# Kernel optimization log

Hardware: AMD Instinct MI355X
Metric: run time of the kernel (lower is better)

Reference implementation:

```python
import jax, jax.numpy as jnp
import numpy as np

N_NODES = 50000
N_EDGES = 800000
IN_DIM = 128
HID = 64
NUM_GRAPHS = 64


def _gcn_conv(x, W, b, src, dst, num_nodes):
    """PyG GCNConv: out = D^-1/2 (A+I) D^-1/2 (x W) + b, messages scattered to dst."""
    h = x @ W  # [N, out]
    ones = jnp.ones((src.shape[0],), dtype=x.dtype)
    # degree at target nodes, self-loop adds 1
    deg = jax.ops.segment_sum(ones, dst, num_segments=num_nodes) + 1.0
    dinv = jax.lax.rsqrt(deg)  # [N]
    norm = dinv[src] * dinv[dst]  # [E]
    msgs = h[src] * norm[:, None]  # [E, out] gather-scale
    agg = jax.ops.segment_sum(msgs, dst, num_segments=num_nodes)  # scatter-add
    # self-loop contribution: norm_ii = dinv[i]^2
    agg = agg + h * (dinv * dinv)[:, None]
    return agg + b


def setup_inputs() -> dict:
    key = jax.random.key(0)
    k = jax.random.split(key, 10)
    x = jax.random.normal(k[0], (N_NODES, IN_DIM), dtype=jnp.float32)
    edge_index = jax.random.randint(k[1], (2, N_EDGES), 0, N_NODES, dtype=jnp.int32)
    batch = jnp.sort(jax.random.randint(k[2], (N_NODES,), 0, NUM_GRAPHS, dtype=jnp.int32))
    # Glorot-ish params
    W1 = jax.random.normal(k[3], (IN_DIM, HID), dtype=jnp.float32) / np.sqrt(IN_DIM)
    b1 = jnp.zeros((HID,), dtype=jnp.float32)
    W2 = jax.random.normal(k[4], (HID, HID), dtype=jnp.float32) / np.sqrt(HID)
    b2 = jnp.zeros((HID,), dtype=jnp.float32)
    Wlin = jax.random.normal(k[5], (HID, 1), dtype=jnp.float32) / np.sqrt(HID)
    blin = jnp.zeros((1,), dtype=jnp.float32)
    return {"x": x, "edge_index": edge_index, "batch": batch,
            "W1": W1, "b1": b1, "W2": W2, "b2": b2, "Wlin": Wlin, "blin": blin}


def reference(x, edge_index, batch, W1, b1, W2, b2, Wlin, blin):
    src, dst = edge_index[0], edge_index[1]
    h = _gcn_conv(x, W1, b1, src, dst, N_NODES)
    h = jax.nn.relu(h)  # dropout is identity in eval mode
    h = _gcn_conv(h, W2, b2, src, dst, N_NODES)
    h = jax.nn.relu(h)
    # global mean pool per graph
    sums = jax.ops.segment_sum(h, batch, num_segments=NUM_GRAPHS)  # [G, HID]
    cnts = jax.ops.segment_sum(jnp.ones((N_NODES,), h.dtype), batch, num_segments=NUM_GRAPHS)
    pooled = sums / jnp.maximum(cnts, 1.0)[:, None]
    return pooled @ Wlin + blin  # [G, 1]
```

## Files before the change

kernel.cpp:

```cpp
#include <hip/hip_runtime.h>
#include <hip/hip_fp16.h>

#define N_NODES 50000
#define N_EDGES 800000
#define IN_DIM 128
#define HID 64
#define NUM_GRAPHS 64
#define NB 196
#define NBLK 64

__device__ inline float4 load_h4(const __half* p) {
    const __half2* q = (const __half2*)p;
    float2 a = __half22float2(q[0]);
    float2 b = __half22float2(q[1]);
    return make_float4(a.x, a.y, b.x, b.y);
}
__device__ inline void store_h4(__half* p, float4 v) {
    __half2* q = (__half2*)p;
    q[0] = __floats2half2_rn(v.x, v.y);
    q[1] = __floats2half2_rn(v.z, v.w);
}
__device__ inline void load_h8(const __half* p, float* f) {
    float4 r = *(const float4*)p;
    const __half2* h = (const __half2*)&r;
    float2 a0 = __half22float2(h[0]);
    float2 a1 = __half22float2(h[1]);
    float2 a2 = __half22float2(h[2]);
    float2 a3 = __half22float2(h[3]);
    f[0] = a0.x; f[1] = a0.y; f[2] = a1.x; f[3] = a1.y;
    f[4] = a2.x; f[5] = a2.y; f[6] = a3.x; f[7] = a3.y;
}
__device__ inline void store_h8(__half* p, const float* f) {
    __half2 hs[4];
    hs[0] = __floats2half2_rn(f[0], f[1]);
    hs[1] = __floats2half2_rn(f[2], f[3]);
    hs[2] = __floats2half2_rn(f[4], f[5]);
    hs[3] = __floats2half2_rn(f[6], f[7]);
    *(float4*)p = *(const float4*)hs;
}

__global__ __launch_bounds__(256) void hist_kernel(const int* __restrict__ dst, int* __restrict__ hist_g) {
    __shared__ int h[NB];
    int tid = threadIdx.x;
    for (int i = tid; i < NB; i += 256) h[i] = 0;
    __syncthreads();
    const int NI = N_EDGES / 4;
    for (int i = blockIdx.x * 256 + tid; i < NI; i += NBLK * 256) {
        int4 d = ((const int4*)dst)[i];
        atomicAdd(&h[d.x >> 8], 1);
        atomicAdd(&h[d.y >> 8], 1);
        atomicAdd(&h[d.z >> 8], 1);
        atomicAdd(&h[d.w >> 8], 1);
    }
    __syncthreads();
    for (int i = tid; i < NB; i += 256) hist_g[i * NBLK + blockIdx.x] = h[i];
}

__global__ __launch_bounds__(1024) void scan2_kernel(const int* __restrict__ in, int* __restrict__ pos,
                                                     int* __restrict__ offs) {
    __shared__ int wsum[16];
    __shared__ int tot_s;
    int tid = threadIdx.x;
    int lane = tid & 63, wid = tid >> 6;
    int carry = 0;
    const int L = NB * NBLK;
    for (int base = 0; base < L; base += 4096) {
        int idx = base + tid * 4;
        int v0 = 0, v1 = 0, v2 = 0, v3 = 0;
        if (idx < L) { int4 v = *(const int4*)&in[idx]; v0 = v.x; v1 = v.y; v2 = v.z; v3 = v.w; }
        int s0 = v0, s1 = s0 + v1, s2 = s1 + v2, s3 = s2 + v3;
        int inc = s3;
        #pragma unroll
        for (int d = 1; d < 64; d <<= 1) { int t = __shfl_up(inc, d, 64); if (lane >= d) inc += t; }
        if (lane == 63) wsum[wid] = inc;
        __syncthreads();
        if (tid < 16) {
            int wv = wsum[tid], winc = wv;
            #pragma unroll
            for (int d = 1; d < 16; d <<= 1) { int t = __shfl_up(winc, d, 16); if (tid >= d) winc += t; }
            wsum[tid] = winc - wv;
            if (tid == 15) tot_s = winc;
        }
        __syncthreads();
        int excl = carry + wsum[wid] + inc - s3;
        if (idx < L) { int4 o; o.x = excl; o.y = excl + s0; o.z = excl + s1; o.w = excl + s2; *(int4*)&pos[idx] = o; }
        carry += tot_s;
    }
    if (tid == 0) offs[N_NODES] = N_EDGES;
}

__global__ __launch_bounds__(256) void bin_kernel(const int* __restrict__ src, const int* __restrict__ dst,
                                                  const int* __restrict__ pos, int* __restrict__ binned) {
    __shared__ int cur[NB];
    int tid = threadIdx.x;
    for (int i = tid; i < NB; i += 256) cur[i] = pos[i * NBLK + blockIdx.x];
    __syncthreads();
    const int NI = N_EDGES / 4;
    for (int i = blockIdx.x * 256 + tid; i < NI; i += NBLK * 256) {
        int4 s = ((const int4*)src)[i];
        int4 d = ((const int4*)dst)[i];
        int p0 = atomicAdd(&cur[d.x >> 8], 1); binned[p0] = (s.x & 0xFFFF) | ((d.x & 255) << 16);
        int p1 = atomicAdd(&cur[d.y >> 8], 1); binned[p1] = (s.y & 0xFFFF) | ((d.y & 255) << 16);
        int p2 = atomicAdd(&cur[d.z >> 8], 1); binned[p2] = (s.z & 0xFFFF) | ((d.z & 255) << 16);
        int p3 = atomicAdd(&cur[d.w >> 8], 1); binned[p3] = (s.w & 0xFFFF) | ((d.w & 255) << 16);
    }
}

__global__ __launch_bounds__(256) void build_kernel(const int* __restrict__ binned, const int* __restrict__ pos,
                                                    int* __restrict__ offs, float* __restrict__ dinv,
                                                    unsigned short* __restrict__ csr_src) {
    __shared__ int cnt[256];
    __shared__ int excl[256];
    __shared__ int rnk[256];
    __shared__ int wtot[4];
    int b = blockIdx.x, tid = threadIdx.x;
    int base = pos[b * NBLK];
    int end  = (b == NB - 1) ? N_EDGES : pos[(b + 1) * NBLK];
    cnt[tid] = 0; rnk[tid] = 0;
    __syncthreads();
    for (int j = base + tid; j < end; j += 256) atomicAdd(&cnt[(binned[j] >> 16) & 255], 1);
    __syncthreads();
    int v = cnt[tid];
    int lane = tid & 63, wid = tid >> 6;
    int inc = v;
    #pragma unroll
    for (int d = 1; d < 64; d <<= 1) { int t = __shfl_up(inc, d, 64); if (lane >= d) inc += t; }
    if (lane == 63) wtot[wid] = inc;
    __syncthreads();
    if (tid == 0) {
        int a = 0;
        for (int w = 0; w < 4; w++) { int t = wtot[w]; wtot[w] = a; a += t; }
    }
    __syncthreads();
    excl[tid] = wtot[wid] + inc - v;
    int node = b * 256 + tid;
    if (node < N_NODES) {
        offs[node] = base + excl[tid];
        dinv[node] = rsqrtf((float)v + 1.0f);
    }
    __syncthreads();
    for (int j = base + tid; j < end; j += 256) {
        int e = binned[j];
        int l = (e >> 16) & 255;
        int r = atomicAdd(&rnk[l], 1);
        csr_src[base + excl[l] + r] = (unsigned short)(e & 0xFFFF);
    }
}

template <int K, typename TIN>
__global__ __launch_bounds__(256) void gemm_kernel(const TIN* __restrict__ A, const float* __restrict__ W,
                                                   const float* __restrict__ dinv,
                                                   __half* __restrict__ out, int nRows) {
    constexpr int KB = 64;
    constexpr int KBP = KB + 4;
    __shared__ float xs[64 * KBP];
    __shared__ float ws[KB * 68];
    int tid = threadIdx.x;
    int node0 = blockIdx.x * 64;
    int c0 = (tid & 15) * 4, n0 = (tid >> 4) * 4;
    float acc[4][4] = {};
    for (int kb = 0; kb < K; kb += KB) {
        for (int i = tid; i < KB * 16; i += 256) {
            int k = i >> 4, c4 = (i & 15) * 4;
            *(float4*)&ws[k * 68 + c4] = *(const float4*)&W[(size_t)(kb + k) * 64 + c4];
        }
        for (int i = tid; i < 64 * (KB / 4); i += 256) {
            int n = i / (KB / 4), k4 = (i % (KB / 4)) * 4;
            int gn = node0 + n;
            float4 v;
            if (gn < nRows) {
                if constexpr (sizeof(TIN) == 4) v = *(const float4*)&A[(size_t)gn * K + kb + k4];
                else                            v = load_h4((const __half*)&A[(size_t)gn * K + kb + k4]);
            } else v = make_float4(0.f, 0.f, 0.f, 0.f);
            *(float4*)&xs[n * KBP + k4] = v;
        }
        __syncthreads();
        for (int k = 0; k < KB; k += 4) {
            float4 x0 = *(const float4*)&xs[(n0 + 0) * KBP + k];
            float4 x1 = *(const float4*)&xs[(n0 + 1) * KBP + k];
            float4 x2 = *(const float4*)&xs[(n0 + 2) * KBP + k];
            float4 x3 = *(const float4*)&xs[(n0 + 3) * KBP + k];
            #define KSTEP(KK, F) { \
                float4 wr = *(const float4*)&ws[(k + KK) * 68 + c0]; \
                acc[0][0] += x0.F * wr.x; acc[0][1] += x0.F * wr.y; acc[0][2] += x0.F * wr.z; acc[0][3] += x0.F * wr.w; \
                acc[1][0] += x1.F * wr.x; acc[1][1] += x1.F * wr.y; acc[1][2] += x1.F * wr.z; acc[1][3] += x1.F * wr.w; \
                acc[2][0] += x2.F * wr.x; acc[2][1] += x2.F * wr.y; acc[2][2] += x2.F * wr.z; acc[2][3] += x2.F * wr.w; \
                acc[3][0] += x3.F * wr.x; acc[3][1] += x3.F * wr.y; acc[3][2] += x3.F * wr.z; acc[3][3] += x3.F * wr.w; }
            KSTEP(0, x)
            KSTEP(1, y)
            KSTEP(2, z)
            KSTEP(3, w)
            #undef KSTEP
        }
        __syncthreads();
    }
    #pragma unroll
    for (int i = 0; i < 4; i++) {
        int gn = node0 + n0 + i;
        if (gn < nRows) {
            float sc = dinv[gn];
            store_h4(&out[(size_t)gn * 64 + c0],
                     make_float4(acc[i][0] * sc, acc[i][1] * sc, acc[i][2] * sc, acc[i][3] * sc));
        }
    }
}

__global__ __launch_bounds__(256) void agg_kernel(const __half* __restrict__ hd, const int* __restrict__ offs,
                                                  const unsigned short* __restrict__ csr_src,
                                                  const float* __restrict__ dinv, const float* __restrict__ bias,
                                                  __half* __restrict__ out) {
    int lane = threadIdx.x & 63;
    int node = blockIdx.x * 4 + (threadIdx.x >> 6);
    if (node >= N_NODES) return;
    int g = lane >> 3;
    int cc = (lane & 7) * 8;
    float acc[8] = {};
    int beg = offs[node], end = offs[node + 1];
    #pragma unroll 2
    for (int j = beg + g; j < end; j += 8) {
        int s = csr_src[j];
        float hv[8];
        load_h8(&hd[(size_t)s * 64 + cc], hv);
        #pragma unroll
        for (int i = 0; i < 8; i++) acc[i] += hv[i];
    }
    #pragma unroll
    for (int m = 8; m <= 32; m <<= 1) {
        #pragma unroll
        for (int i = 0; i < 8; i++) acc[i] += __shfl_xor(acc[i], m, 64);
    }
    if (g == 0) {
        float di = dinv[node];
        float hn[8];
        load_h8(&hd[(size_t)node * 64 + cc], hn);
        float4 bv0 = *(const float4*)&bias[cc];
        float4 bv1 = *(const float4*)&bias[cc + 4];
        float bb[8] = {bv0.x, bv0.y, bv0.z, bv0.w, bv1.x, bv1.y, bv1.z, bv1.w};
        float r[8];
        #pragma unroll
        for (int i = 0; i < 8; i++) r[i] = fmaxf(fmaf(di, acc[i] + hn[i], bb[i]), 0.0f);
        store_h8(&out[(size_t)node * 64 + cc], r);
    }
}

__global__ __launch_bounds__(256) void agg2dot_kernel(const __half* __restrict__ hd, const int* __restrict__ offs,
                                                      const unsigned short* __restrict__ csr_src,
                                                      const float* __restrict__ dinv, const float* __restrict__ bias,
                                                      const float* __restrict__ Wlin,
                                                      float* __restrict__ ndot) {
    int lane = threadIdx.x & 63;
    int node = blockIdx.x * 4 + (threadIdx.x >> 6);
    if (node >= N_NODES) return;
    int g = lane >> 3;
    int cc = (lane & 7) * 8;
    float acc[8] = {};
    int beg = offs[node], end = offs[node + 1];
    #pragma unroll 2
    for (int j = beg + g; j < end; j += 8) {
        int s = csr_src[j];
        float hv[8];
        load_h8(&hd[(size_t)s * 64 + cc], hv);
        #pragma unroll
        for (int i = 0; i < 8; i++) acc[i] += hv[i];
    }
    #pragma unroll
    for (int m = 8; m <= 32; m <<= 1) {
        #pragma unroll
        for (int i = 0; i < 8; i++) acc[i] += __shfl_xor(acc[i], m, 64);
    }
    if (g == 0) {
        float di = dinv[node];
        float hn[8];
        load_h8(&hd[(size_t)node * 64 + cc], hn);
        float4 bv0 = *(const float4*)&bias[cc];
        float4 bv1 = *(const float4*)&bias[cc + 4];
        float bb[8] = {bv0.x, bv0.y, bv0.z, bv0.w, bv1.x, bv1.y, bv1.z, bv1.w};
        float4 wl0 = *(const float4*)&Wlin[cc];
        float4 wl1 = *(const float4*)&Wlin[cc + 4];
        float ww[8] = {wl0.x, wl0.y, wl0.z, wl0.w, wl1.x, wl1.y, wl1.z, wl1.w};
        float d = 0.0f;
        #pragma unroll
        for (int i = 0; i < 8; i++) {
            float r = fmaxf(fmaf(di, acc[i] + hn[i], bb[i]), 0.0f);
            d = fmaf(r, ww[i], d);
        }
        #pragma unroll
        for (int m = 1; m < 8; m <<= 1) d += __shfl_xor(d, m, 64);
        if ((lane & 7) == 0) ndot[node] = d;
    }
}

__global__ __launch_bounds__(256) void graphred_kernel(const float* __restrict__ ndot, const int* __restrict__ batch,
                                                       const float* __restrict__ blin, float* __restrict__ out) {
    __shared__ float wpart[4];
    int g = blockIdx.x;
    int tid = threadIdx.x;
    int lo = 0, hi = N_NODES;
    while (lo < hi) { int m = (lo + hi) >> 1; if (batch[m] < g) lo = m + 1; else hi = m; }
    int lo2 = lo, hi2 = N_NODES;
    while (lo2 < hi2) { int m = (lo2 + hi2) >> 1; if (batch[m] < g + 1) lo2 = m + 1; else hi2 = m; }
    float s = 0.0f;
    for (int i = lo + tid; i < lo2; i += 256) s += ndot[i];
    int lane = tid & 63, wid = tid >> 6;
    #pragma unroll
    for (int m = 32; m > 0; m >>= 1) s += __shfl_down(s, m, 64);
    if (lane == 0) wpart[wid] = s;
    __syncthreads();
    if (tid == 0) {
        float t = wpart[0] + wpart[1] + wpart[2] + wpart[3];
        float cnt = (float)(lo2 - lo);
        out[g] = t / fmaxf(cnt, 1.0f) + blin[0];
    }
}

extern "C" void kernel_launch(void* const* d_in, const int* in_sizes, int n_in,
                              void* d_out, int out_size, void* d_ws, size_t ws_size,
                              hipStream_t stream) {
    const float* x    = (const float*)d_in[0];
    const int*   ei   = (const int*)d_in[1];
    const int*   batch= (const int*)d_in[2];
    const float* W1   = (const float*)d_in[3];
    const float* b1   = (const float*)d_in[4];
    const float* W2   = (const float*)d_in[5];
    const float* b2   = (const float*)d_in[6];
    const float* Wlin = (const float*)d_in[7];
    const float* blin = (const float*)d_in[8];
    float* out = (float*)d_out;
    const int* srcA = ei;
    const int* dstA = ei + N_EDGES;

    char* p = (char*)d_ws;
    auto alloc = [&](size_t n) { char* r = p; p += (n + 255) & ~(size_t)255; return r; };
    int*    hist_g  = (int*)alloc((size_t)NB * NBLK * 4);
    int*    pos     = (int*)alloc((size_t)NB * NBLK * 4);
    int*    offs    = (int*)alloc((size_t)(N_NODES + 1) * 4);
    int*    binned  = (int*)alloc((size_t)N_EDGES * 4);
    unsigned short* csr_src = (unsigned short*)alloc((size_t)N_EDGES * 2);
    float*  dinv    = (float*)alloc((size_t)N_NODES * 4);
    float*  ndot    = (float*)alloc((size_t)N_NODES * 4);
    __half* bufA    = (__half*)alloc((size_t)N_NODES * 64 * 2);
    __half* bufB    = (__half*)alloc((size_t)N_NODES * 64 * 2);

    hist_kernel<<<NBLK, 256, 0, stream>>>(dstA, hist_g);
    scan2_kernel<<<1, 1024, 0, stream>>>(hist_g, pos, offs);
    bin_kernel<<<NBLK, 256, 0, stream>>>(srcA, dstA, pos, binned);
    build_kernel<<<NB, 256, 0, stream>>>(binned, pos, offs, dinv, csr_src);

    gemm_kernel<IN_DIM, float><<<(N_NODES + 63) / 64, 256, 0, stream>>>(x, W1, dinv, bufA, N_NODES);
    agg_kernel<<<(N_NODES + 3) / 4, 256, 0, stream>>>(bufA, offs, csr_src, dinv, b1, bufB);
    gemm_kernel<HID, __half><<<(N_NODES + 63) / 64, 256, 0, stream>>>(bufB, W2, dinv, bufA, N_NODES);
    agg2dot_kernel<<<(N_NODES + 3) / 4, 256, 0, stream>>>(bufA, offs, csr_src, dinv, b2, Wlin, ndot);

    graphred_kernel<<<NUM_GRAPHS, 256, 0, stream>>>(ndot, batch, blin, out);
}
```

Baseline: 206.8 us.

## Fuse graph-build, GEMM1, scan/bin and pooling kernels to cut launches

Runs the dst histogram, the per-graph node counts and the first GEMM as branches of one kernel, dropping the dinv pre-scaling so GEMM1 no longer waits on the degree build; dinv[src] is applied per edge in the first aggregation instead. Each of the 64 binning blocks now computes the full hist scan redundantly in shared memory, which removes the single-block scan launch. Graph pooling moves into the second aggregation kernel through slotted float atomics and a last-block-arrives reduction, which removes the separate graph-reduction kernel. The costs are an extra per-edge dinv gather, a 50 KB shared-memory load in every binning block, and atomic contention on the pooling slots.

```diff
diff --git a/kernel.cpp b/kernel.cpp
--- a/kernel.cpp
+++ b/kernel.cpp
@@ -8,6 +8,7 @@
 #define NUM_GRAPHS 64
 #define NB 196
 #define NBLK 64
+#define NSLOT 32
 
 __device__ inline float4 load_h4(const __half* p) {
     const __half2* q = (const __half2*)p;
@@ -39,147 +40,34 @@
     *(float4*)p = *(const float4*)hs;
 }
 
-__global__ __launch_bounds__(256) void hist_kernel(const int* __restrict__ dst, int* __restrict__ hist_g) {
-    __shared__ int h[NB];
+template <int K, typename TIN, bool SCALE>
+__device__ __forceinline__ void gemm_body(const TIN* __restrict__ A, const float* __restrict__ W,
+                                          const float* __restrict__ dinv, __half* __restrict__ out,
+                                          int nRows, int node0, float* xs, float* ws) {
     int tid = threadIdx.x;
-    for (int i = tid; i < NB; i += 256) h[i] = 0;
-    __syncthreads();
-    const int NI = N_EDGES / 4;
-    for (int i = blockIdx.x * 256 + tid; i < NI; i += NBLK * 256) {
-        int4 d = ((const int4*)dst)[i];
-        atomicAdd(&h[d.x >> 8], 1);
-        atomicAdd(&h[d.y >> 8], 1);
-        atomicAdd(&h[d.z >> 8], 1);
-        atomicAdd(&h[d.w >> 8], 1);
-    }
-    __syncthreads();
-    for (int i = tid; i < NB; i += 256) hist_g[i * NBLK + blockIdx.x] = h[i];
-}
-
-__global__ __launch_bounds__(1024) void scan2_kernel(const int* __restrict__ in, int* __restrict__ pos,
-                                                     int* __restrict__ offs) {
-    __shared__ int wsum[16];
-    __shared__ int tot_s;
-    int tid = threadIdx.x;
-    int lane = tid & 63, wid = tid >> 6;
-    int carry = 0;
-    const int L = NB * NBLK;
-    for (int base = 0; base < L; base += 4096) {
-        int idx = base + tid * 4;
-        int v0 = 0, v1 = 0, v2 = 0, v3 = 0;
-        if (idx < L) { int4 v = *(const int4*)&in[idx]; v0 = v.x; v1 = v.y; v2 = v.z; v3 = v.w; }
-        int s0 = v0, s1 = s0 + v1, s2 = s1 + v2, s3 = s2 + v3;
-        int inc = s3;
-        #pragma unroll
-        for (int d = 1; d < 64; d <<= 1) { int t = __shfl_up(inc, d, 64); if (lane >= d) inc += t; }
-        if (lane == 63) wsum[wid] = inc;
-        __syncthreads();
-        if (tid < 16) {
-            int wv = wsum[tid], winc = wv;
-            #pragma unroll
-            for (int d = 1; d < 16; d <<= 1) { int t = __shfl_up(winc, d, 16); if (tid >= d) winc += t; }
-            wsum[tid] = winc - wv;
-            if (tid == 15) tot_s = winc;
-        }
-        __syncthreads();
-        int excl = carry + wsum[wid] + inc - s3;
-        if (idx < L) { int4 o; o.x = excl; o.y = excl + s0; o.z = excl + s1; o.w = excl + s2; *(int4*)&pos[idx] = o; }
-        carry += tot_s;
-    }
-    if (tid == 0) offs[N_NODES] = N_EDGES;
-}
-
-__global__ __launch_bounds__(256) void bin_kernel(const int* __restrict__ src, const int* __restrict__ dst,
-                                                  const int* __restrict__ pos, int* __restrict__ binned) {
-    __shared__ int cur[NB];
-    int tid = threadIdx.x;
-    for (int i = tid; i < NB; i += 256) cur[i] = pos[i * NBLK + blockIdx.x];
-    __syncthreads();
-    const int NI = N_EDGES / 4;
-    for (int i = blockIdx.x * 256 + tid; i < NI; i += NBLK * 256) {
-        int4 s = ((const int4*)src)[i];
-        int4 d = ((const int4*)dst)[i];
-        int p0 = atomicAdd(&cur[d.x >> 8], 1); binned[p0] = (s.x & 0xFFFF) | ((d.x & 255) << 16);
-        int p1 = atomicAdd(&cur[d.y >> 8], 1); binned[p1] = (s.y & 0xFFFF) | ((d.y & 255) << 16);
-        int p2 = atomicAdd(&cur[d.z >> 8], 1); binned[p2] = (s.z & 0xFFFF) | ((d.z & 255) << 16);
-        int p3 = atomicAdd(&cur[d.w >> 8], 1); binned[p3] = (s.w & 0xFFFF) | ((d.w & 255) << 16);
-    }
-}
-
-__global__ __launch_bounds__(256) void build_kernel(const int* __restrict__ binned, const int* __restrict__ pos,
-                                                    int* __restrict__ offs, float* __restrict__ dinv,
-                                                    unsigned short* __restrict__ csr_src) {
-    __shared__ int cnt[256];
-    __shared__ int excl[256];
-    __shared__ int rnk[256];
-    __shared__ int wtot[4];
-    int b = blockIdx.x, tid = threadIdx.x;
-    int base = pos[b * NBLK];
-    int end  = (b == NB - 1) ? N_EDGES : pos[(b + 1) * NBLK];
-    cnt[tid] = 0; rnk[tid] = 0;
-    __syncthreads();
-    for (int j = base + tid; j < end; j += 256) atomicAdd(&cnt[(binned[j] >> 16) & 255], 1);
-    __syncthreads();
-    int v = cnt[tid];
-    int lane = tid & 63, wid = tid >> 6;
-    int inc = v;
-    #pragma unroll
-    for (int d = 1; d < 64; d <<= 1) { int t = __shfl_up(inc, d, 64); if (lane >= d) inc += t; }
-    if (lane == 63) wtot[wid] = inc;
-    __syncthreads();
-    if (tid == 0) {
-        int a = 0;
-        for (int w = 0; w < 4; w++) { int t = wtot[w]; wtot[w] = a; a += t; }
-    }
-    __syncthreads();
-    excl[tid] = wtot[wid] + inc - v;
-    int node = b * 256 + tid;
-    if (node < N_NODES) {
-        offs[node] = base + excl[tid];
-        dinv[node] = rsqrtf((float)v + 1.0f);
-    }
-    __syncthreads();
-    for (int j = base + tid; j < end; j += 256) {
-        int e = binned[j];
-        int l = (e >> 16) & 255;
-        int r = atomicAdd(&rnk[l], 1);
-        csr_src[base + excl[l] + r] = (unsigned short)(e & 0xFFFF);
-    }
-}
-
-template <int K, typename TIN>
-__global__ __launch_bounds__(256) void gemm_kernel(const TIN* __restrict__ A, const float* __restrict__ W,
-                                                   const float* __restrict__ dinv,
-                                                   __half* __restrict__ out, int nRows) {
-    constexpr int KB = 64;
-    constexpr int KBP = KB + 4;
-    __shared__ float xs[64 * KBP];
-    __shared__ float ws[KB * 68];
-    int tid = threadIdx.x;
-    int node0 = blockIdx.x * 64;
     int c0 = (tid & 15) * 4, n0 = (tid >> 4) * 4;
     float acc[4][4] = {};
-    for (int kb = 0; kb < K; kb += KB) {
-        for (int i = tid; i < KB * 16; i += 256) {
+    for (int kb = 0; kb < K; kb += 64) {
+        for (int i = tid; i < 64 * 16; i += 256) {
             int k = i >> 4, c4 = (i & 15) * 4;
             *(float4*)&ws[k * 68 + c4] = *(const float4*)&W[(size_t)(kb + k) * 64 + c4];
         }
-        for (int i = tid; i < 64 * (KB / 4); i += 256) {
-            int n = i / (KB / 4), k4 = (i % (KB / 4)) * 4;
+        for (int i = tid; i < 64 * 16; i += 256) {
+            int n = i >> 4, k4 = (i & 15) * 4;
             int gn = node0 + n;
             float4 v;
             if (gn < nRows) {
                 if constexpr (sizeof(TIN) == 4) v = *(const float4*)&A[(size_t)gn * K + kb + k4];
                 else                            v = load_h4((const __half*)&A[(size_t)gn * K + kb + k4]);
             } else v = make_float4(0.f, 0.f, 0.f, 0.f);
-            *(float4*)&xs[n * KBP + k4] = v;
-        }
-        __syncthreads();
-        for (int k = 0; k < KB; k += 4) {
-            float4 x0 = *(const float4*)&xs[(n0 + 0) * KBP + k];
-            float4 x1 = *(const float4*)&xs[(n0 + 1) * KBP + k];
-            float4 x2 = *(const float4*)&xs[(n0 + 2) * KBP + k];
-            float4 x3 = *(const float4*)&xs[(n0 + 3) * KBP + k];
+            *(float4*)&xs[n * 68 + k4] = v;
+        }
+        __syncthreads();
+        for (int k = 0; k < 64; k += 4) {
+            float4 x0 = *(const float4*)&xs[(n0 + 0) * 68 + k];
+            float4 x1 = *(const float4*)&xs[(n0 + 1) * 68 + k];
+            float4 x2 = *(const float4*)&xs[(n0 + 2) * 68 + k];
+            float4 x3 = *(const float4*)&xs[(n0 + 3) * 68 + k];
             #define KSTEP(KK, F) { \
                 float4 wr = *(const float4*)&ws[(k + KK) * 68 + c0]; \
                 acc[0][0] += x0.F * wr.x; acc[0][1] += x0.F * wr.y; acc[0][2] += x0.F * wr.z; acc[0][3] += x0.F * wr.w; \
@@ -198,20 +86,147 @@
     for (int i = 0; i < 4; i++) {
         int gn = node0 + n0 + i;
         if (gn < nRows) {
-            float sc = dinv[gn];
+            float sc = 1.0f;
+            if constexpr (SCALE) sc = dinv[gn];
             store_h4(&out[(size_t)gn * 64 + c0],
                      make_float4(acc[i][0] * sc, acc[i][1] * sc, acc[i][2] * sc, acc[i][3] * sc));
         }
     }
 }
 
-__global__ __launch_bounds__(256) void agg_kernel(const __half* __restrict__ hd, const int* __restrict__ offs,
-                                                  const unsigned short* __restrict__ csr_src,
-                                                  const float* __restrict__ dinv, const float* __restrict__ bias,
-                                                  __half* __restrict__ out) {
+__global__ __launch_bounds__(256) void k1_kernel(const int* __restrict__ dst, int* __restrict__ hist_g,
+                                                 const float* __restrict__ x, const float* __restrict__ W1,
+                                                 __half* __restrict__ h1,
+                                                 const int* __restrict__ batch, float* __restrict__ gsum,
+                                                 int* __restrict__ gcnt, int* __restrict__ arrive) {
+    __shared__ __align__(16) float smem[2 * 64 * 68];
+    int blk = blockIdx.x, tid = threadIdx.x;
+    if (blk < NBLK) {
+        int* h = (int*)smem;
+        for (int i = tid; i < NB; i += 256) h[i] = 0;
+        __syncthreads();
+        const int NI = N_EDGES / 4;
+        for (int i = blk * 256 + tid; i < NI; i += NBLK * 256) {
+            int4 d = ((const int4*)dst)[i];
+            atomicAdd(&h[d.x >> 8], 1);
+            atomicAdd(&h[d.y >> 8], 1);
+            atomicAdd(&h[d.z >> 8], 1);
+            atomicAdd(&h[d.w >> 8], 1);
+        }
+        __syncthreads();
+        for (int i = tid; i < NB; i += 256) hist_g[i * NBLK + blk] = h[i];
+    } else if (blk == NBLK) {
+        int* c = (int*)smem;
+        if (tid < NUM_GRAPHS) c[tid] = 0;
+        for (int i = tid; i < NSLOT * NUM_GRAPHS; i += 256) gsum[i] = 0.0f;
+        if (tid == 0) arrive[0] = 0;
+        __syncthreads();
+        const int4* b4 = (const int4*)batch;
+        for (int i = tid; i < N_NODES / 4; i += 256) {
+            int4 v = b4[i];
+            atomicAdd(&c[v.x], 1); atomicAdd(&c[v.y], 1);
+            atomicAdd(&c[v.z], 1); atomicAdd(&c[v.w], 1);
+        }
+        __syncthreads();
+        if (tid < NUM_GRAPHS) gcnt[tid] = c[tid];
+    } else {
+        int node0 = (blk - NBLK - 1) * 64;
+        gemm_body<IN_DIM, float, false>(x, W1, nullptr, h1, N_NODES, node0, smem, smem + 64 * 68);
+    }
+}
+
+__global__ __launch_bounds__(256) void k2_binscan(const int* __restrict__ hist_g,
+                                                  const int* __restrict__ src, const int* __restrict__ dst,
+                                                  int* __restrict__ binned, int* __restrict__ bstart,
+                                                  int* __restrict__ offs) {
+    __shared__ int ld[NB * NBLK];
+    __shared__ int cur[NB];
+    __shared__ int wsum[4];
+    int tid = threadIdx.x, blk = blockIdx.x;
+    for (int i = tid; i < NB * NBLK; i += 256) ld[i] = hist_g[i];
+    __syncthreads();
+    const int CH = (NB * NBLK) / 256;
+    int base = tid * CH;
+    int s = 0;
+    for (int k = 0; k < CH; k++) { int v = ld[base + k]; ld[base + k] = s; s += v; }
+    int lane = tid & 63, wid = tid >> 6;
+    int inc = s;
+    #pragma unroll
+    for (int d = 1; d < 64; d <<= 1) { int t = __shfl_up(inc, d, 64); if (lane >= d) inc += t; }
+    if (lane == 63) wsum[wid] = inc;
+    __syncthreads();
+    if (tid == 0) {
+        int a = 0;
+        for (int w = 0; w < 4; w++) { int t = wsum[w]; wsum[w] = a; a += t; }
+    }
+    __syncthreads();
+    int off = wsum[wid] + inc - s;
+    for (int k = 0; k < CH; k++) ld[base + k] += off;
+    __syncthreads();
+    for (int b = tid; b < NB; b += 256) cur[b] = ld[b * NBLK + blk];
+    if (blk == 0) {
+        for (int b = tid; b < NB; b += 256) bstart[b] = ld[b * NBLK];
+        if (tid == 0) { bstart[NB] = N_EDGES; offs[N_NODES] = N_EDGES; }
+    }
+    __syncthreads();
+    const int NI = N_EDGES / 4;
+    for (int i = blk * 256 + tid; i < NI; i += NBLK * 256) {
+        int4 sv = ((const int4*)src)[i];
+        int4 dv = ((const int4*)dst)[i];
+        int p0 = atomicAdd(&cur[dv.x >> 8], 1); binned[p0] = (sv.x & 0xFFFF) | ((dv.x & 255) << 16);
+        int p1 = atomicAdd(&cur[dv.y >> 8], 1); binned[p1] = (sv.y & 0xFFFF) | ((dv.y & 255) << 16);
+        int p2 = atomicAdd(&cur[dv.z >> 8], 1); binned[p2] = (sv.z & 0xFFFF) | ((dv.z & 255) << 16);
+        int p3 = atomicAdd(&cur[dv.w >> 8], 1); binned[p3] = (sv.w & 0xFFFF) | ((dv.w & 255) << 16);
+    }
+}
+
+__global__ __launch_bounds__(256) void build_kernel(const int* __restrict__ binned, const int* __restrict__ bstart,
+                                                    int* __restrict__ offs, float* __restrict__ dinv,
+                                                    unsigned short* __restrict__ csr_src) {
+    __shared__ int cnt[256];
+    __shared__ int excl[256];
+    __shared__ int rnk[256];
+    __shared__ int wtot[4];
+    int b = blockIdx.x, tid = threadIdx.x;
+    int base = bstart[b];
+    int end  = bstart[b + 1];
+    cnt[tid] = 0; rnk[tid] = 0;
+    __syncthreads();
+    for (int j = base + tid; j < end; j += 256) atomicAdd(&cnt[(binned[j] >> 16) & 255], 1);
+    __syncthreads();
+    int v = cnt[tid];
+    int lane = tid & 63, wid = tid >> 6;
+    int inc = v;
+    #pragma unroll
+    for (int d = 1; d < 64; d <<= 1) { int t = __shfl_up(inc, d, 64); if (lane >= d) inc += t; }
+    if (lane == 63) wtot[wid] = inc;
+    __syncthreads();
+    if (tid == 0) {
+        int a = 0;
+        for (int w = 0; w < 4; w++) { int t = wtot[w]; wtot[w] = a; a += t; }
+    }
+    __syncthreads();
+    excl[tid] = wtot[wid] + inc - v;
+    int node = b * 256 + tid;
+    if (node < N_NODES) {
+        offs[node] = base + excl[tid];
+        dinv[node] = rsqrtf((float)v + 1.0f);
+    }
+    __syncthreads();
+    for (int j = base + tid; j < end; j += 256) {
+        int e = binned[j];
+        int l = (e >> 16) & 255;
+        int r = atomicAdd(&rnk[l], 1);
+        csr_src[base + excl[l] + r] = (unsigned short)(e & 0xFFFF);
+    }
+}
+
+__global__ __launch_bounds__(256) void agg1_kernel(const __half* __restrict__ hd, const int* __restrict__ offs,
+                                                   const unsigned short* __restrict__ csr_src,
+                                                   const float* __restrict__ dinv, const float* __restrict__ bias,
+                                                   __half* __restrict__ out) {
     int lane = threadIdx.x & 63;
     int node = blockIdx.x * 4 + (threadIdx.x >> 6);
-    if (node >= N_NODES) return;
     int g = lane >> 3;
     int cc = (lane & 7) * 8;
     float acc[8] = {};
@@ -219,10 +234,11 @@
     #pragma unroll 2
     for (int j = beg + g; j < end; j += 8) {
         int s = csr_src[j];
+        float dv = dinv[s];
         float hv[8];
         load_h8(&hd[(size_t)s * 64 + cc], hv);
         #pragma unroll
-        for (int i = 0; i < 8; i++) acc[i] += hv[i];
+        for (int i = 0; i < 8; i++) acc[i] = fmaf(hv[i], dv, acc[i]);
     }
     #pragma unroll
     for (int m = 8; m <= 32; m <<= 1) {
@@ -231,6 +247,7 @@
     }
     if (g == 0) {
         float di = dinv[node];
+        float d2 = di * di;
         float hn[8];
         load_h8(&hd[(size_t)node * 64 + cc], hn);
         float4 bv0 = *(const float4*)&bias[cc];
@@ -238,19 +255,27 @@
         float bb[8] = {bv0.x, bv0.y, bv0.z, bv0.w, bv1.x, bv1.y, bv1.z, bv1.w};
         float r[8];
         #pragma unroll
-        for (int i = 0; i < 8; i++) r[i] = fmaxf(fmaf(di, acc[i] + hn[i], bb[i]), 0.0f);
+        for (int i = 0; i < 8; i++) r[i] = fmaxf(fmaf(di, acc[i], fmaf(d2, hn[i], bb[i])), 0.0f);
         store_h8(&out[(size_t)node * 64 + cc], r);
     }
 }
 
-__global__ __launch_bounds__(256) void agg2dot_kernel(const __half* __restrict__ hd, const int* __restrict__ offs,
+__global__ __launch_bounds__(256) void gemm2_kernel(const __half* __restrict__ A, const float* __restrict__ W,
+                                                    const float* __restrict__ dinv, __half* __restrict__ out) {
+    __shared__ __align__(16) float smem[2 * 64 * 68];
+    gemm_body<HID, __half, true>(A, W, dinv, out, N_NODES, blockIdx.x * 64, smem, smem + 64 * 68);
+}
+
+__global__ __launch_bounds__(256) void agg2red_kernel(const __half* __restrict__ hd, const int* __restrict__ offs,
                                                       const unsigned short* __restrict__ csr_src,
                                                       const float* __restrict__ dinv, const float* __restrict__ bias,
-                                                      const float* __restrict__ Wlin,
-                                                      float* __restrict__ ndot) {
+                                                      const float* __restrict__ Wlin, const int* __restrict__ batch,
+                                                      float* __restrict__ gsum, const int* __restrict__ gcnt,
+                                                      int* __restrict__ arrive, const float* __restrict__ blin,
+                                                      float* __restrict__ out) {
+    __shared__ int is_last;
     int lane = threadIdx.x & 63;
     int node = blockIdx.x * 4 + (threadIdx.x >> 6);
-    if (node >= N_NODES) return;
     int g = lane >> 3;
     int cc = (lane & 7) * 8;
     float acc[8] = {};
@@ -286,30 +311,25 @@
         }
         #pragma unroll
         for (int m = 1; m < 8; m <<= 1) d += __shfl_xor(d, m, 64);
-        if ((lane & 7) == 0) ndot[node] = d;
-    }
-}
-
-__global__ __launch_bounds__(256) void graphred_kernel(const float* __restrict__ ndot, const int* __restrict__ batch,
-                                                       const float* __restrict__ blin, float* __restrict__ out) {
-    __shared__ float wpart[4];
-    int g = blockIdx.x;
-    int tid = threadIdx.x;
-    int lo = 0, hi = N_NODES;
-    while (lo < hi) { int m = (lo + hi) >> 1; if (batch[m] < g) lo = m + 1; else hi = m; }
-    int lo2 = lo, hi2 = N_NODES;
-    while (lo2 < hi2) { int m = (lo2 + hi2) >> 1; if (batch[m] < g + 1) lo2 = m + 1; else hi2 = m; }
-    float s = 0.0f;
-    for (int i = lo + tid; i < lo2; i += 256) s += ndot[i];
-    int lane = tid & 63, wid = tid >> 6;
-    #pragma unroll
-    for (int m = 32; m > 0; m >>= 1) s += __shfl_down(s, m, 64);
-    if (lane == 0) wpart[wid] = s;
-    __syncthreads();
-    if (tid == 0) {
-        float t = wpart[0] + wpart[1] + wpart[2] + wpart[3];
-        float cnt = (float)(lo2 - lo);
-        out[g] = t / fmaxf(cnt, 1.0f) + blin[0];
+        if (lane == 0) {
+            int gb = batch[node];
+            atomicAdd(&gsum[(blockIdx.x & (NSLOT - 1)) * NUM_GRAPHS + gb], d);
+        }
+    }
+    __syncthreads();
+    if (threadIdx.x == 0) {
+        __threadfence();
+        int old = atomicAdd(arrive, 1);
+        is_last = (old == (int)gridDim.x - 1) ? 1 : 0;
+    }
+    __syncthreads();
+    if (is_last && threadIdx.x < NUM_GRAPHS) {
+        int gg = threadIdx.x;
+        float s = 0.0f;
+        #pragma unroll
+        for (int slot = 0; slot < NSLOT; slot++) s += atomicAdd(&gsum[slot * NUM_GRAPHS + gg], 0.0f);
+        float cnt = (float)gcnt[gg];
+        out[gg] = s / fmaxf(cnt, 1.0f) + blin[0];
     }
 }
 
@@ -332,24 +352,24 @@
     char* p = (char*)d_ws;
     auto alloc = [&](size_t n) { char* r = p; p += (n + 255) & ~(size_t)255; return r; };
     int*    hist_g  = (int*)alloc((size_t)NB * NBLK * 4);
-    int*    pos     = (int*)alloc((size_t)NB * NBLK * 4);
+    int*    bstart  = (int*)alloc((size_t)(NB + 1) * 4);
     int*    offs    = (int*)alloc((size_t)(N_NODES + 1) * 4);
     int*    binned  = (int*)alloc((size_t)N_EDGES * 4);
     unsigned short* csr_src = (unsigned short*)alloc((size_t)N_EDGES * 2);
     float*  dinv    = (float*)alloc((size_t)N_NODES * 4);
-    float*  ndot    = (float*)alloc((size_t)N_NODES * 4);
+    float*  gsum    = (float*)alloc((size_t)NSLOT * NUM_GRAPHS * 4);
+    int*    gcnt    = (int*)alloc((size_t)NUM_GRAPHS * 4);
+    int*    arrive  = (int*)alloc(4);
     __half* bufA    = (__half*)alloc((size_t)N_NODES * 64 * 2);
     __half* bufB    = (__half*)alloc((size_t)N_NODES * 64 * 2);
 
-    hist_kernel<<<NBLK, 256, 0, stream>>>(dstA, hist_g);
-    scan2_kernel<<<1, 1024, 0, stream>>>(hist_g, pos, offs);
-    bin_kernel<<<NBLK, 256, 0, stream>>>(srcA, dstA, pos, binned);
-    build_kernel<<<NB, 256, 0, stream>>>(binned, pos, offs, dinv, csr_src);
-
-    gemm_kernel<IN_DIM, float><<<(N_NODES + 63) / 64, 256, 0, stream>>>(x, W1, dinv, bufA, N_NODES);
-    agg_kernel<<<(N_NODES + 3) / 4, 256, 0, stream>>>(bufA, offs, csr_src, dinv, b1, bufB);
-    gemm_kernel<HID, __half><<<(N_NODES + 63) / 64, 256, 0, stream>>>(bufB, W2, dinv, bufA, N_NODES);
-    agg2dot_kernel<<<(N_NODES + 3) / 4, 256, 0, stream>>>(bufA, offs, csr_src, dinv, b2, Wlin, ndot);
-
-    graphred_kernel<<<NUM_GRAPHS, 256, 0, stream>>>(ndot, batch, blin, out);
-}
+    const int GEMM1_BLOCKS = (N_NODES + 63) / 64;
+    k1_kernel<<<NBLK + 1 + GEMM1_BLOCKS, 256, 0, stream>>>(dstA, hist_g, x, W1, bufA,
+                                                           batch, gsum, gcnt, arrive);
+    k2_binscan<<<NBLK, 256, 0, stream>>>(hist_g, srcA, dstA, binned, bstart, offs);
+    build_kernel<<<NB, 256, 0, stream>>>(binned, bstart, offs, dinv, csr_src);
+    agg1_kernel<<<N_NODES / 4, 256, 0, stream>>>(bufA, offs, csr_src, dinv, b1, bufB);
+    gemm2_kernel<<<GEMM1_BLOCKS, 256, 0, stream>>>(bufB, W2, dinv, bufA);
+    agg2red_kernel<<<N_NODES / 4, 256, 0, stream>>>(bufA, offs, csr_src, dinv, b2, Wlin, batch,
+                                                    gsum, gcnt, arrive, blin, out);
+}
```

After: 499.5 us. +141.6%, slower.
